# Optimization experiments

Measured on AMD Instinct MI355X. Metric: run time of the kernel, lower is better.

The kernel has to match this reference:

```python
import jax, jax.numpy as jnp
import numpy as np

N_NODES = 50000
N_EDGES = 1_600_000
IN_F = 128
OUT_F = 32
HEADS = 4
EDGE_F = 4
EDGE_HID = 32


def setup_inputs() -> dict:
    key = jax.random.key(0)
    ks = jax.random.split(key, 12)
    x = jax.random.normal(ks[0], (N_NODES, IN_F), dtype=jnp.float32)
    edge_index = jax.random.randint(ks[1], (2, N_EDGES), 0, N_NODES, dtype=jnp.int32)
    edge_attr = jax.random.normal(ks[2], (N_EDGES, EDGE_F), dtype=jnp.float32)
    # linear: in_features -> heads*out_features (stored as [in, out] for x @ W)
    W = jax.random.normal(ks[3], (IN_F, HEADS * OUT_F), dtype=jnp.float32) * (1.0 / np.sqrt(IN_F))
    b = jnp.zeros((HEADS * OUT_F,), dtype=jnp.float32)
    # edge_proj: Linear(EDGE_F,32) -> ReLU -> Linear(32, heads)
    eW1 = jax.random.normal(ks[4], (EDGE_F, EDGE_HID), dtype=jnp.float32) * (1.0 / np.sqrt(EDGE_F))
    eb1 = jnp.zeros((EDGE_HID,), dtype=jnp.float32)
    eW2 = jax.random.normal(ks[5], (EDGE_HID, HEADS), dtype=jnp.float32) * (1.0 / np.sqrt(EDGE_HID))
    eb2 = jnp.zeros((HEADS,), dtype=jnp.float32)
    att_src = jax.random.normal(ks[6], (1, HEADS, OUT_F), dtype=jnp.float32) * 0.1
    att_dst = jax.random.normal(ks[7], (1, HEADS, OUT_F), dtype=jnp.float32) * 0.1
    return {"x": x, "edge_index": edge_index, "edge_attr": edge_attr,
            "W": W, "b": b, "eW1": eW1, "eb1": eb1, "eW2": eW2, "eb2": eb2,
            "att_src": att_src, "att_dst": att_dst}


def reference(x, edge_index, edge_attr, W, b, eW1, eb1, eW2, eb2, att_src, att_dst):
    N = x.shape[0]
    src, dst = edge_index[0], edge_index[1]
    E = src.shape[0]

    h = (x @ W + b).reshape(N, HEADS, OUT_F)                     # [N,H,F]
    alpha_src = jnp.sum(h[src] * att_src, axis=-1)               # [E,H]
    alpha_dst = jnp.sum(h[dst] * att_dst, axis=-1)               # [E,H]
    edge_att = jax.nn.relu(edge_attr @ eW1 + eb1) @ eW2 + eb2    # [E,H]
    alpha = jax.nn.leaky_relu(alpha_src + alpha_dst + edge_att, negative_slope=0.2)

    # softmax_by_src: dense [N,H] buffer of -inf, scatter-set by src
    # softmax over the NODE axis, then gather back per edge.
    last = jax.ops.segment_max(jnp.arange(E, dtype=jnp.int32), src, num_segments=N)  # [N]
    valid = last >= 0
    dense = jnp.where(valid[:, None], alpha[jnp.clip(last, 0)], -jnp.inf)  # [N,H]
    dense = jax.nn.softmax(dense, axis=0)
    alpha_e = dense[src]                                         # [E,H]

    # dropout: module default training=False path (identity), eval mode
    # scatter-add aggregation: out[src] += h[dst] * alpha_e (all heads at once)
    msg = h[dst] * alpha_e[:, :, None]                           # [E,H,F]
    out = jnp.zeros_like(h).at[src].add(msg)                     # [N,H,F]
    return out.mean(axis=1)                                      # [N,F]
```

## Files before the change

### kernel.cpp

```cpp
#include <hip/hip_runtime.h>
#include <hip/hip_fp16.h>
#include <math.h>


#define SUPCAP 9216
#define AGG_CAP 2048
#define BIN_CHUNK 2048

__global__ __launch_bounds__(256, 3) void k_pre(
    const float* __restrict__ x, const float* __restrict__ W,
    const float* __restrict__ b, const float* __restrict__ att_src,
    const float* __restrict__ att_dst, __half* __restrict__ hbuf16,
    float* __restrict__ s_, float* __restrict__ t_,
    const int* __restrict__ src, const int* __restrict__ dst,
    int* __restrict__ bcur, uint2* __restrict__ bin2,
    int N, int E, int nsup, int ngemm, int nbin) {
  __shared__ __align__(16) float smem[12672];
  int tx = threadIdx.x;
  int bid = blockIdx.x;
  int mmin = (nbin < ngemm) ? nbin : ngemm;
  int m2 = 2 * mmin;
  bool isbin;
  int wid;
  if (bid < m2) { isbin = (bid & 1); wid = bid >> 1; }
  else { isbin = (nbin > ngemm); wid = mmin + (bid - m2); }

  if (isbin) {
    uint2* ebuf = (uint2*)smem;
    int* hist = (int*)(smem + 4096);
    int* bas  = hist + 256;
    int* curs = bas + 256;
    int* gpos = curs + 256;
    int e0 = wid * BIN_CHUNK;
    int n = E - e0; if (n > BIN_CHUNK) n = BIN_CHUNK;
    hist[tx] = 0;
    __syncthreads();
    for (int i = tx; i < n; i += 256) {
      atomicAdd(&hist[src[e0 + i] >> 8], 1);
    }
    __syncthreads();
    int v = hist[tx];
    bas[tx] = v;
    __syncthreads();
    for (int off = 1; off < 256; off <<= 1) {
      int t = (tx >= off) ? bas[tx - off] : 0;
      __syncthreads();
      bas[tx] += t;
      __syncthreads();
    }
    curs[tx] = bas[tx] - v;
    if (tx < nsup && v > 0) gpos[tx] = atomicAdd(&bcur[tx], v);
    __syncthreads();
    for (int i = tx; i < n; i += 256) {
      int e = e0 + i;
      int s = src[e], d = dst[e];
      int pos = atomicAdd(&curs[s >> 8], 1);
      unsigned loc = (unsigned)(s & 255);
      ebuf[pos] = make_uint2((loc << 24) | (unsigned)e, (loc << 16) | (unsigned)d);
    }
    __syncthreads();
    for (int i = tx; i < n; i += 256) {
      uint2 w = ebuf[i];
      int lo = 0, hi = 255;
      while (lo < hi) {
        int mid = (lo + hi) >> 1;
        if (bas[mid] > i) hi = mid; else lo = mid + 1;
      }
      int bb = lo;
      int lbase = bas[bb] - hist[bb];
      int off = gpos[bb] + (i - lbase);
      if (off < SUPCAP) {
        bin2[(size_t)bb * SUPCAP + off] = w;
      }
    }
  } else {
    float* xs = smem;
    float* ws = smem + 64 * 132;
    int r0 = wid * 64;
    const float4* xg = (const float4*)(x + (size_t)r0 * 128);
#pragma unroll
    for (int j = 0; j < 8; ++j) {
      int l = tx + j * 256;
      int row = l >> 5, col4 = l & 31;
      float4 v = make_float4(0.f, 0.f, 0.f, 0.f);
      if (r0 + row < N) v = xg[l];
      *(float4*)(xs + row * 132 + col4 * 4) = v;
    }
    int cg = tx & 15, rg = tx >> 4;
    float acc[4][8];
#pragma unroll
    for (int r = 0; r < 4; ++r)
#pragma unroll
      for (int c = 0; c < 8; ++c) acc[r][c] = 0.f;
    const float4* Wg4 = (const float4*)W;
    const float* xbase = xs + rg * 4 * 132;
    int woff = cg * 8 + ((cg >> 3) << 2);
    for (int kt = 0; kt < 4; ++kt) {
      __syncthreads();
#pragma unroll
      for (int j = 0; j < 4; ++j) {
        int ll = tx + j * 256;
        int row = ll >> 5, c4 = ll & 31;
        *(float4*)(ws + row * 132 + c4 * 4 + ((c4 >> 4) << 2)) = Wg4[kt * 1024 + ll];
      }
      __syncthreads();
#pragma unroll 2
      for (int k4 = 0; k4 < 8; ++k4) {
        float4 xr0 = *(const float4*)(xbase + kt * 32 + k4 * 4);
        float4 xr1 = *(const float4*)(xbase + 132 + kt * 32 + k4 * 4);
        float4 xr2 = *(const float4*)(xbase + 264 + kt * 32 + k4 * 4);
        float4 xr3 = *(const float4*)(xbase + 396 + kt * 32 + k4 * 4);
#pragma unroll
        for (int kk = 0; kk < 4; ++kk) {
          const float* wrow = ws + (k4 * 4 + kk) * 132 + woff;
          float4 w0 = *(const float4*)(wrow);
          float4 w1 = *(const float4*)(wrow + 4);
          const float wc[8] = {w0.x, w0.y, w0.z, w0.w, w1.x, w1.y, w1.z, w1.w};
          float xv0 = ((const float*)&xr0)[kk];
          float xv1 = ((const float*)&xr1)[kk];
          float xv2 = ((const float*)&xr2)[kk];
          float xv3 = ((const float*)&xr3)[kk];
#pragma unroll
          for (int c = 0; c < 8; ++c) {
            acc[0][c] += xv0 * wc[c];
            acc[1][c] += xv1 * wc[c];
            acc[2][c] += xv2 * wc[c];
            acc[3][c] += xv3 * wc[c];
          }
        }
      }
    }
    float4 b0 = ((const float4*)b)[cg * 2],       b1 = ((const float4*)b)[cg * 2 + 1];
    float4 s0 = ((const float4*)att_src)[cg * 2], s1 = ((const float4*)att_src)[cg * 2 + 1];
    float4 d0 = ((const float4*)att_dst)[cg * 2], d1 = ((const float4*)att_dst)[cg * 2 + 1];
    const float bbv[8] = {b0.x, b0.y, b0.z, b0.w, b1.x, b1.y, b1.z, b1.w};
    const float asv[8] = {s0.x, s0.y, s0.z, s0.w, s1.x, s1.y, s1.z, s1.w};
    const float adv[8] = {d0.x, d0.y, d0.z, d0.w, d1.x, d1.y, d1.z, d1.w};
    int hd = cg >> 2;
#pragma unroll
    for (int r = 0; r < 4; ++r) {
      float o[8];
#pragma unroll
      for (int c = 0; c < 8; ++c) o[c] = acc[r][c] + bbv[c];
      float sp = 0.f, tp = 0.f;
#pragma unroll
      for (int c = 0; c < 8; ++c) { sp += o[c] * asv[c]; tp += o[c] * adv[c]; }
      sp += __shfl_xor(sp, 1); sp += __shfl_xor(sp, 2);
      tp += __shfl_xor(tp, 1); tp += __shfl_xor(tp, 2);
      int grow = r0 + rg * 4 + r;
      if (grow < N) {
        __half2 h0 = __floats2half2_rn(o[0], o[1]);
        __half2 h1 = __floats2half2_rn(o[2], o[3]);
        __half2 h2 = __floats2half2_rn(o[4], o[5]);
        __half2 h3 = __floats2half2_rn(o[6], o[7]);
        uint4 u;
        u.x = *(unsigned*)&h0; u.y = *(unsigned*)&h1;
        u.z = *(unsigned*)&h2; u.w = *(unsigned*)&h3;
        ((uint4*)(hbuf16 + (size_t)grow * 128))[cg] = u;
        if ((tx & 3) == 0) {
          s_[grow * 4 + hd] = sp;
          t_[grow * 4 + hd] = tp;
        }
      }
    }
  }
}

__global__ __launch_bounds__(1024, 1) void k_dense(
    const int* __restrict__ bcur, const uint2* __restrict__ bin2,
    const int* __restrict__ dst, const float* __restrict__ edge_attr,
    const float* __restrict__ eW1, const float* __restrict__ eb1,
    const float* __restrict__ eW2, const float* __restrict__ eb2,
    const float* __restrict__ s_, const float* __restrict__ t_,
    float* __restrict__ dense, float* __restrict__ pmax,
    float* __restrict__ psum,
    unsigned short* __restrict__ sorted_dst,
    int* __restrict__ noff, int* __restrict__ ncnt, int N) {
  __shared__ int lastv[256];
  __shared__ int hist[256], bas[256], curs[256];
  __shared__ float lm[256 * 4], ls[256 * 4];
  int sp = blockIdx.x, tx = threadIdx.x;
  if (tx < 256) { lastv[tx] = -1; hist[tx] = 0; }
  __syncthreads();
  int cnt = bcur[sp]; if (cnt > SUPCAP) cnt = SUPCAP;
  const uint2* b2 = bin2 + (size_t)sp * SUPCAP;
  for (int i = tx; i < cnt; i += 1024) {
    uint2 w = b2[i];
    atomicMax(&lastv[w.x >> 24], (int)(w.x & 0xFFFFFF));
    atomicAdd(&hist[w.y >> 16], 1);
  }
  __syncthreads();
  int v = 0;
  if (tx < 256) { v = hist[tx]; bas[tx] = v; }
  __syncthreads();
  for (int off = 1; off < 256; off <<= 1) {
    int t = 0;
    if (tx < 256 && tx >= off) t = bas[tx - off];
    __syncthreads();
    if (tx < 256) bas[tx] += t;
    __syncthreads();
  }
  int gn = sp * 256 + tx;
  if (tx < 256) {
    curs[tx] = bas[tx] - v;
    noff[gn] = sp * SUPCAP + bas[tx] - v;
    ncnt[gn] = v;
  }
  __syncthreads();
  unsigned short* sd = sorted_dst + (size_t)sp * SUPCAP;
  for (int i = tx; i < cnt; i += 1024) {
    unsigned y = b2[i].y;
    int pos = atomicAdd(&curs[y >> 16], 1);
    sd[pos] = (unsigned short)y;
  }
  float vv[4] = {-INFINITY, -INFINITY, -INFINITY, -INFINITY};
  if (tx < 256 && gn < N) {
    int e = lastv[tx];
    if (e >= 0) {
      int d = dst[e];
      const float* ea = edge_attr + (size_t)e * 4;
      float e0 = ea[0], e1 = ea[1], e2 = ea[2], e3 = ea[3];
      float a0 = eb2[0], a1 = eb2[1], a2 = eb2[2], a3 = eb2[3];
#pragma unroll
      for (int i = 0; i < 32; ++i) {
        float hid = eb1[i] + e0 * eW1[i] + e1 * eW1[32 + i] + e2 * eW1[64 + i] + e3 * eW1[96 + i];
        hid = fmaxf(hid, 0.f);
        a0 += hid * eW2[i * 4 + 0]; a1 += hid * eW2[i * 4 + 1];
        a2 += hid * eW2[i * 4 + 2]; a3 += hid * eW2[i * 4 + 3];
      }
      float w0 = s_[gn * 4 + 0] + t_[d * 4 + 0] + a0;
      float w1 = s_[gn * 4 + 1] + t_[d * 4 + 1] + a1;
      float w2 = s_[gn * 4 + 2] + t_[d * 4 + 2] + a2;
      float w3 = s_[gn * 4 + 3] + t_[d * 4 + 3] + a3;
      vv[0] = w0 > 0.f ? w0 : 0.2f * w0;
      vv[1] = w1 > 0.f ? w1 : 0.2f * w1;
      vv[2] = w2 > 0.f ? w2 : 0.2f * w2;
      vv[3] = w3 > 0.f ? w3 : 0.2f * w3;
    }
#pragma unroll
    for (int h = 0; h < 4; ++h) dense[gn * 4 + h] = vv[h];
  }
  if (tx < 256) {
#pragma unroll
    for (int h = 0; h < 4; ++h) {
      lm[tx * 4 + h] = vv[h];
      ls[tx * 4 + h] = (vv[h] > -INFINITY) ? 1.f : 0.f;
    }
  }
  __syncthreads();
  for (int off = 128; off > 0; off >>= 1) {
    if (tx < off) {
#pragma unroll
      for (int h = 0; h < 4; ++h) {
        float m2 = lm[(tx + off) * 4 + h], s2 = ls[(tx + off) * 4 + h];
        float m1 = lm[tx * 4 + h], s1 = ls[tx * 4 + h];
        float M = fmaxf(m1, m2);
        if (M > -INFINITY) {
          ls[tx * 4 + h] = s1 * expf(m1 - M) + s2 * expf(m2 - M);
          lm[tx * 4 + h] = M;
        }
      }
    }
    __syncthreads();
  }
  if (tx == 0) {
#pragma unroll
    for (int h = 0; h < 4; ++h) {
      pmax[sp * 4 + h] = lm[h];
      psum[sp * 4 + h] = ls[h];
    }
  }
}

#define ACC(r, P, Q) { \
  float2 f0 = __half22float2(*(__half2*)&r.x), f1 = __half22float2(*(__half2*)&r.y); \
  float2 f2 = __half22float2(*(__half2*)&r.z), f3 = __half22float2(*(__half2*)&r.w); \
  P.x += f0.x; P.y += f0.y; P.z += f1.x; P.w += f1.y; \
  Q.x += f2.x; Q.y += f2.y; Q.z += f3.x; Q.w += f3.y; }

__global__ __launch_bounds__(256) void k_agg(
    const unsigned short* __restrict__ sorted_dst,
    const int* __restrict__ noff, const int* __restrict__ ncnt,
    const __half* __restrict__ hbuf16, const float* __restrict__ dense,
    const float* __restrict__ pmax, const float* __restrict__ psum, int nb,
    float* __restrict__ out, int N) {
  __shared__ unsigned short sl[AGG_CAP];
  __shared__ float lm[256], ls[256];
  __shared__ float sgm[4], sgi[4];
  int tx = threadIdx.x;
  int n0 = blockIdx.x << 4;
  int nlast = n0 + 15; if (nlast > N - 1) nlast = N - 1;
  int lstart = noff[n0];
  int lend = noff[nlast] + ncnt[nlast];
  int total = lend - lstart; if (total > AGG_CAP) total = AGG_CAP;
  for (int i = tx; i < total; i += 256) sl[i] = sorted_dst[lstart + i];
  {
    int h = tx & 3, chunk = tx >> 2;
    float m = -INFINITY, s = 0.f;
    for (int bq = chunk; bq < nb; bq += 64) {
      float m2 = pmax[bq * 4 + h], s2 = psum[bq * 4 + h];
      float M = fmaxf(m, m2);
      if (M > -INFINITY) {
        s = s * expf(m - M) + s2 * expf(m2 - M);
        m = M;
      }
    }
    lm[tx] = m; ls[tx] = s;
    __syncthreads();
    for (int off = 128; off >= 4; off >>= 1) {
      if (tx < off) {
        float m2 = lm[tx + off], s2 = ls[tx + off];
        float m1 = lm[tx], s1 = ls[tx];
        float M = fmaxf(m1, m2);
        if (M > -INFINITY) {
          ls[tx] = s1 * expf(m1 - M) + s2 * expf(m2 - M);
          lm[tx] = M;
        }
      }
      __syncthreads();
    }
    if (tx < 4) {
      sgm[tx] = lm[tx];
      sgi[tx] = 1.f / ls[tx];
    }
    __syncthreads();
  }
  int g = tx >> 4, l = tx & 15;
  int n = n0 + g;
  if (n >= N) return;
  int beg = noff[n] - lstart;
  int cnt = ncnt[n];
  if (beg + cnt > total) cnt = total - beg;
  int end = beg + cnt;
  int hd = l >> 2;
  float w = expf(dense[(size_t)n * 4 + hd] - sgm[hd]) * sgi[hd];
  float4 p0 = {0, 0, 0, 0}, q0 = {0, 0, 0, 0};
  float4 p1 = {0, 0, 0, 0}, q1 = {0, 0, 0, 0};
  int e = beg;
  for (; e + 7 < end; e += 8) {
    int c0 = sl[e],     c1 = sl[e + 1], c2 = sl[e + 2], c3 = sl[e + 3];
    int c4_ = sl[e + 4], c5 = sl[e + 5], c6 = sl[e + 6], c7 = sl[e + 7];
    uint4 r0 = *((const uint4*)(hbuf16 + ((size_t)c0  << 7)) + l);
    uint4 r1 = *((const uint4*)(hbuf16 + ((size_t)c1  << 7)) + l);
    uint4 r2 = *((const uint4*)(hbuf16 + ((size_t)c2  << 7)) + l);
    uint4 r3 = *((const uint4*)(hbuf16 + ((size_t)c3  << 7)) + l);
    uint4 r4 = *((const uint4*)(hbuf16 + ((size_t)c4_ << 7)) + l);
    uint4 r5 = *((const uint4*)(hbuf16 + ((size_t)c5  << 7)) + l);
    uint4 r6 = *((const uint4*)(hbuf16 + ((size_t)c6  << 7)) + l);
    uint4 r7 = *((const uint4*)(hbuf16 + ((size_t)c7  << 7)) + l);
    ACC(r0, p0, q0); ACC(r1, p1, q1); ACC(r2, p0, q0); ACC(r3, p1, q1);
    ACC(r4, p0, q0); ACC(r5, p1, q1); ACC(r6, p0, q0); ACC(r7, p1, q1);
  }
  for (; e + 3 < end; e += 4) {
    int c0 = sl[e], c1 = sl[e + 1], c2 = sl[e + 2], c3 = sl[e + 3];
    uint4 r0 = *((const uint4*)(hbuf16 + ((size_t)c0 << 7)) + l);
    uint4 r1 = *((const uint4*)(hbuf16 + ((size_t)c1 << 7)) + l);
    uint4 r2 = *((const uint4*)(hbuf16 + ((size_t)c2 << 7)) + l);
    uint4 r3 = *((const uint4*)(hbuf16 + ((size_t)c3 << 7)) + l);
    ACC(r0, p0, q0); ACC(r1, p1, q1); ACC(r2, p0, q0); ACC(r3, p1, q1);
  }
  for (; e < end; ++e) {
    int c0 = sl[e];
    uint4 r0 = *((const uint4*)(hbuf16 + ((size_t)c0 << 7)) + l);
    ACC(r0, p0, q0);
  }
  p0.x += p1.x; p0.y += p1.y; p0.z += p1.z; p0.w += p1.w;
  q0.x += q1.x; q0.y += q1.y; q0.z += q1.z; q0.w += q1.w;
  p0.x *= w; p0.y *= w; p0.z *= w; p0.w *= w;
  q0.x *= w; q0.y *= w; q0.z *= w; q0.w *= w;
  p0.x += __shfl_xor(p0.x, 4);  p0.y += __shfl_xor(p0.y, 4);
  p0.z += __shfl_xor(p0.z, 4);  p0.w += __shfl_xor(p0.w, 4);
  q0.x += __shfl_xor(q0.x, 4);  q0.y += __shfl_xor(q0.y, 4);
  q0.z += __shfl_xor(q0.z, 4);  q0.w += __shfl_xor(q0.w, 4);
  p0.x += __shfl_xor(p0.x, 8);  p0.y += __shfl_xor(p0.y, 8);
  p0.z += __shfl_xor(p0.z, 8);  p0.w += __shfl_xor(p0.w, 8);
  q0.x += __shfl_xor(q0.x, 8);  q0.y += __shfl_xor(q0.y, 8);
  q0.z += __shfl_xor(q0.z, 8);  q0.w += __shfl_xor(q0.w, 8);
  if (l < 4) {
    float4 oA, oB;
    oA.x = 0.25f * p0.x; oA.y = 0.25f * p0.y; oA.z = 0.25f * p0.z; oA.w = 0.25f * p0.w;
    oB.x = 0.25f * q0.x; oB.y = 0.25f * q0.y; oB.z = 0.25f * q0.z; oB.w = 0.25f * q0.w;
    *(float4*)(out + (size_t)n * 32 + l * 8) = oA;
    *(float4*)(out + (size_t)n * 32 + l * 8 + 4) = oB;
  }
}

extern "C" void kernel_launch(void* const* d_in, const int* in_sizes, int n_in,
                              void* d_out, int out_size, void* d_ws, size_t ws_size,
                              hipStream_t stream) {
  const float* x        = (const float*)d_in[0];
  const int*   ei       = (const int*)d_in[1];
  const float* edge_attr= (const float*)d_in[2];
  const float* W        = (const float*)d_in[3];
  const float* b        = (const float*)d_in[4];
  const float* eW1      = (const float*)d_in[5];
  const float* eb1      = (const float*)d_in[6];
  const float* eW2      = (const float*)d_in[7];
  const float* eb2      = (const float*)d_in[8];
  const float* att_src  = (const float*)d_in[9];
  const float* att_dst  = (const float*)d_in[10];
  float* out = (float*)d_out;

  const int N = in_sizes[0] / 128;
  const int E = in_sizes[1] / 2;
  const int* src = ei;
  const int* dst = ei + E;
  const int NSUP = (N + 255) >> 8;

  char* wp = (char*)d_ws;
  auto alloc = [&](size_t bytes) -> void* {
    void* p = (void*)wp;
    wp += (bytes + 255) & ~(size_t)255;
    return p;
  };
  __half* hbuf16 = (__half*)alloc((size_t)N * 128 * 2);
  float* s_    = (float*)alloc((size_t)N * 4 * 4);
  float* t_    = (float*)alloc((size_t)N * 4 * 4);
  float* dense = (float*)alloc((size_t)N * 4 * 4);
  float* pmax  = (float*)alloc((size_t)NSUP * 4 * 4);
  float* psum  = (float*)alloc((size_t)NSUP * 4 * 4);
  int* bcur    = (int*)alloc((size_t)NSUP * 4);
  uint2* bin2  = (uint2*)alloc((size_t)NSUP * SUPCAP * 8);
  unsigned short* sorted_dst = (unsigned short*)alloc((size_t)NSUP * SUPCAP * 2);
  int* noff    = (int*)alloc((size_t)NSUP * 256 * 4);
  int* ncnt    = (int*)alloc((size_t)NSUP * 256 * 4);

  const int NGEMM = (N + 63) / 64;
  const int NBIN  = (E + BIN_CHUNK - 1) / BIN_CHUNK;

  hipMemsetAsync(bcur, 0, (size_t)NSUP * 4, stream);
  k_pre<<<NGEMM + NBIN, 256, 0, stream>>>(x, W, b, att_src, att_dst, hbuf16, s_, t_,
                                          src, dst, bcur, bin2,
                                          N, E, NSUP, NGEMM, NBIN);
  k_dense<<<NSUP, 1024, 0, stream>>>(bcur, bin2, dst, edge_attr, eW1, eb1, eW2, eb2,
                                     s_, t_, dense, pmax, psum, sorted_dst, noff, ncnt, N);
  k_agg<<<(N + 15) / 16, 256, 0, stream>>>(sorted_dst, noff, ncnt, hbuf16, dense,
                                           pmax, psum, NSUP, out, N);
}
```

Measured before the change: 224.4 us.

## Precompute bin offsets, split edge MLP across lanes, widen aggregation blocks

In the binning path, each edge's destination bin and global offset are now recorded when the edge is placed in shared memory. The scatter loop reads that record instead of running a 256-entry binary search. The dense kernel now computes the last-edge MLP with 4 threads per node over a 1024-thread block, each thread doing 8 of the 32 hidden units and combining results with xor shuffles, where before only 256 of the 1024 threads did the work. The aggregation kernel moves to 512-thread blocks covering 32 nodes, and its shared list capacity grows to match. These changes add shared-memory use and shuffle work in exchange for removing serial search and idle threads. Any change to k_agg's inner mapping falls in the lines not shown, so full consistency cannot be verified.

```diff
diff --git a/kernel.cpp b/kernel.cpp
--- a/kernel.cpp
+++ b/kernel.cpp
@@ -4,7 +4,7 @@
 
 
 #define SUPCAP 9216
-#define AGG_CAP 2048
+#define AGG_CAP 4096
 #define BIN_CHUNK 2048
 
 __global__ __launch_bounds__(256, 3) void k_pre(
@@ -27,10 +27,12 @@
 
   if (isbin) {
     uint2* ebuf = (uint2*)smem;
-    int* hist = (int*)(smem + 4096);
+    int* obo  = (int*)(smem + 4096);
+    int* hist = (int*)(smem + 6144);
     int* bas  = hist + 256;
     int* curs = bas + 256;
     int* gpos = curs + 256;
+    int* gofs = gpos + 256;
     int e0 = wid * BIN_CHUNK;
     int n = E - e0; if (n > BIN_CHUNK) n = BIN_CHUNK;
     hist[tx] = 0;
@@ -48,30 +50,30 @@
       bas[tx] += t;
       __syncthreads();
     }
-    curs[tx] = bas[tx] - v;
-    if (tx < nsup && v > 0) gpos[tx] = atomicAdd(&bcur[tx], v);
+    int lbase = bas[tx] - v;
+    curs[tx] = lbase;
+    int gp = 0;
+    if (tx < nsup && v > 0) gp = atomicAdd(&bcur[tx], v);
+    gpos[tx] = gp;
+    gofs[tx] = gp - lbase;
     __syncthreads();
     for (int i = tx; i < n; i += 256) {
       int e = e0 + i;
       int s = src[e], d = dst[e];
-      int pos = atomicAdd(&curs[s >> 8], 1);
+      int bb = s >> 8;
+      int pos = atomicAdd(&curs[bb], 1);
       unsigned loc = (unsigned)(s & 255);
       ebuf[pos] = make_uint2((loc << 24) | (unsigned)e, (loc << 16) | (unsigned)d);
+      int offb = gofs[bb] + pos;
+      obo[pos] = (offb << 8) | bb;
     }
     __syncthreads();
     for (int i = tx; i < n; i += 256) {
       uint2 w = ebuf[i];
-      int lo = 0, hi = 255;
-      while (lo < hi) {
-        int mid = (lo + hi) >> 1;
-        if (bas[mid] > i) hi = mid; else lo = mid + 1;
-      }
-      int bb = lo;
-      int lbase = bas[bb] - hist[bb];
-      int off = gpos[bb] + (i - lbase);
-      if (off < SUPCAP) {
-        bin2[(size_t)bb * SUPCAP + off] = w;
-      }
+      int ob = obo[i];
+      int bb = ob & 255;
+      int offb = ob >> 8;
+      if (offb < SUPCAP) bin2[(size_t)bb * SUPCAP + offb] = w;
     }
   } else {
     float* xs = smem;
@@ -200,8 +202,8 @@
     if (tx < 256) bas[tx] += t;
     __syncthreads();
   }
-  int gn = sp * 256 + tx;
   if (tx < 256) {
+    int gn = sp * 256 + tx;
     curs[tx] = bas[tx] - v;
     noff[gn] = sp * SUPCAP + bas[tx] - v;
     ncnt[gn] = v;
@@ -213,38 +215,50 @@
     int pos = atomicAdd(&curs[y >> 16], 1);
     sd[pos] = (unsigned short)y;
   }
+  int node = tx >> 2, sub = tx & 3;
+  int gn2 = sp * 256 + node;
   float vv[4] = {-INFINITY, -INFINITY, -INFINITY, -INFINITY};
-  if (tx < 256 && gn < N) {
-    int e = lastv[tx];
-    if (e >= 0) {
+  {
+    int e = lastv[node];
+    if (e >= 0 && gn2 < N) {
       int d = dst[e];
       const float* ea = edge_attr + (size_t)e * 4;
       float e0 = ea[0], e1 = ea[1], e2 = ea[2], e3 = ea[3];
-      float a0 = eb2[0], a1 = eb2[1], a2 = eb2[2], a3 = eb2[3];
-#pragma unroll
-      for (int i = 0; i < 32; ++i) {
+      float a0 = 0.f, a1 = 0.f, a2 = 0.f, a3 = 0.f;
+#pragma unroll
+      for (int j = 0; j < 8; ++j) {
+        int i = sub * 8 + j;
         float hid = eb1[i] + e0 * eW1[i] + e1 * eW1[32 + i] + e2 * eW1[64 + i] + e3 * eW1[96 + i];
         hid = fmaxf(hid, 0.f);
         a0 += hid * eW2[i * 4 + 0]; a1 += hid * eW2[i * 4 + 1];
         a2 += hid * eW2[i * 4 + 2]; a3 += hid * eW2[i * 4 + 3];
       }
-      float w0 = s_[gn * 4 + 0] + t_[d * 4 + 0] + a0;
-      float w1 = s_[gn * 4 + 1] + t_[d * 4 + 1] + a1;
-      float w2 = s_[gn * 4 + 2] + t_[d * 4 + 2] + a2;
-      float w3 = s_[gn * 4 + 3] + t_[d * 4 + 3] + a3;
-      vv[0] = w0 > 0.f ? w0 : 0.2f * w0;
-      vv[1] = w1 > 0.f ? w1 : 0.2f * w1;
-      vv[2] = w2 > 0.f ? w2 : 0.2f * w2;
-      vv[3] = w3 > 0.f ? w3 : 0.2f * w3;
-    }
-#pragma unroll
-    for (int h = 0; h < 4; ++h) dense[gn * 4 + h] = vv[h];
-  }
-  if (tx < 256) {
+      a0 += __shfl_xor(a0, 1); a0 += __shfl_xor(a0, 2);
+      a1 += __shfl_xor(a1, 1); a1 += __shfl_xor(a1, 2);
+      a2 += __shfl_xor(a2, 1); a2 += __shfl_xor(a2, 2);
+      a3 += __shfl_xor(a3, 1); a3 += __shfl_xor(a3, 2);
+      if (sub == 0) {
+        a0 += eb2[0]; a1 += eb2[1]; a2 += eb2[2]; a3 += eb2[3];
+        float w0 = s_[gn2 * 4 + 0] + t_[d * 4 + 0] + a0;
+        float w1 = s_[gn2 * 4 + 1] + t_[d * 4 + 1] + a1;
+        float w2 = s_[gn2 * 4 + 2] + t_[d * 4 + 2] + a2;
+        float w3 = s_[gn2 * 4 + 3] + t_[d * 4 + 3] + a3;
+        vv[0] = w0 > 0.f ? w0 : 0.2f * w0;
+        vv[1] = w1 > 0.f ? w1 : 0.2f * w1;
+        vv[2] = w2 > 0.f ? w2 : 0.2f * w2;
+        vv[3] = w3 > 0.f ? w3 : 0.2f * w3;
+      }
+    }
+  }
+  if (sub == 0) {
+    if (gn2 < N) {
+#pragma unroll
+      for (int h = 0; h < 4; ++h) dense[gn2 * 4 + h] = vv[h];
+    }
 #pragma unroll
     for (int h = 0; h < 4; ++h) {
-      lm[tx * 4 + h] = vv[h];
-      ls[tx * 4 + h] = (vv[h] > -INFINITY) ? 1.f : 0.f;
+      lm[node * 4 + h] = vv[h];
+      ls[node * 4 + h] = (vv[h] > -INFINITY) ? 1.f : 0.f;
     }
   }
   __syncthreads();
@@ -278,26 +292,26 @@
   P.x += f0.x; P.y += f0.y; P.z += f1.x; P.w += f1.y; \
   Q.x += f2.x; Q.y += f2.y; Q.z += f3.x; Q.w += f3.y; }
 
-__global__ __launch_bounds__(256) void k_agg(
+__global__ __launch_bounds__(512) void k_agg(
     const unsigned short* __restrict__ sorted_dst,
     const int* __restrict__ noff, const int* __restrict__ ncnt,
     const __half* __restrict__ hbuf16, const float* __restrict__ dense,
     const float* __restrict__ pmax, const float* __restrict__ psum, int nb,
     float* __restrict__ out, int N) {
   __shared__ unsigned short sl[AGG_CAP];
-  __shared__ float lm[256], ls[256];
+  __shared__ float lm[512], ls[512];
   __shared__ float sgm[4], sgi[4];
   int tx = threadIdx.x;
-  int n0 = blockIdx.x << 4;
-  int nlast = n0 + 15; if (nlast > N - 1) nlast = N - 1;
+  int n0 = blockIdx.x << 5;
+  int nlast = n0 + 31; if (nlast > N - 1) nlast = N - 1;
   int lstart = noff[n0];
   int lend = noff[nlast] + ncnt[nlast];
   int total = lend - lstart; if (total > AGG_CAP) total = AGG_CAP;
-  for (int i = tx; i < total; i += 256) sl[i] = sorted_dst[lstart + i];
+  for (int i = tx; i < total; i += 512) sl[i] = sorted_dst[lstart + i];
   {
     int h = tx & 3, chunk = tx >> 2;
     float m = -INFINITY, s = 0.f;
-    for (int bq = chunk; bq < nb; bq += 64) {
+    for (int bq = chunk; bq < nb; bq += 128) {
       float m2 = pmax[bq * 4 + h], s2 = psum[bq * 4 + h];
       float M = fmaxf(m, m2);
       if (M > -INFINITY) {
@@ -307,7 +321,7 @@
     }
     lm[tx] = m; ls[tx] = s;
     __syncthreads();
-    for (int off = 128; off >= 4; off >>= 1) {
+    for (int off = 256; off >= 4; off >>= 1) {
       if (tx < off) {
         float m2 = lm[tx + off], s2 = ls[tx + off];
         float m1 = lm[tx], s1 = ls[tx];
@@ -434,6 +448,6 @@
                                           N, E, NSUP, NGEMM, NBIN);
   k_dense<<<NSUP, 1024, 0, stream>>>(bcur, bin2, dst, edge_attr, eW1, eb1, eW2, eb2,
                                      s_, t_, dense, pmax, psum, sorted_dst, noff, ncnt, N);
-  k_agg<<<(N + 15) / 16, 256, 0, stream>>>(sorted_dst, noff, ncnt, hbuf16, dense,
+  k_agg<<<(N + 31) / 32, 512, 0, stream>>>(sorted_dst, noff, ncnt, hbuf16, dense,
                                            pmax, psum, NSUP, out, N);
 }
```

Result: slower. 235.1 us (+4.7%).
